# Kernel optimization log

Hardware: AMD Instinct MI355X
Metric: run time of the kernel (lower is better)

Reference implementation:

```python
import jax, jax.numpy as jnp
import numpy as np

N_NODES = 50000
N_EDGES = 250000
N_GRAPHS = 512
F_IN = 32
F_EDGE = 16
LATENT = 32
EMBED = 128


def setup_inputs() -> dict:
    key = jax.random.key(0)
    ks = jax.random.split(key, 10)
    x = jax.random.normal(ks[0], (N_NODES, F_IN), dtype=jnp.float32)
    edge_index = jax.random.randint(ks[1], (2, N_EDGES), 0, N_NODES, dtype=jnp.int64)
    edge_attr = jax.random.normal(ks[2], (N_EDGES, F_EDGE), dtype=jnp.float32)
    batch = jnp.sort(jax.random.randint(ks[3], (N_NODES,), 0, N_GRAPHS, dtype=jnp.int64))
    s = 0.05
    W1 = jax.random.normal(ks[4], (F_EDGE, LATENT), dtype=jnp.float32) * s
    b1 = jnp.zeros((LATENT,), jnp.float32)
    W2 = jax.random.normal(ks[5], (LATENT, F_IN * LATENT), dtype=jnp.float32) * s
    b2 = jnp.zeros((F_IN * LATENT,), jnp.float32)
    root = jax.random.normal(ks[6], (F_IN, LATENT), dtype=jnp.float32) * s
    conv_bias = jnp.zeros((LATENT,), jnp.float32)
    fc_w = jax.random.normal(ks[7], (LATENT, EMBED), dtype=jnp.float32) * s
    fc_b = jnp.zeros((EMBED,), jnp.float32)
    return dict(x=x, edge_index=edge_index, edge_attr=edge_attr, batch=batch,
                W1=W1, b1=b1, W2=W2, b2=b2, root=root, conv_bias=conv_bias,
                fc_w=fc_w, fc_b=fc_b)


def reference(x, edge_index, edge_attr, batch, W1, b1, W2, b2, root, conv_bias, fc_w, fc_b):
    src, dst = edge_index[0], edge_index[1]
    # edge MLP: [E, F_edge] -> [E, F_in*latent] -> [E, F_in, latent]
    h = jax.nn.relu(edge_attr @ W1 + b1)
    ew = (h @ W2 + b2).reshape(-1, F_IN, LATENT)
    # per-edge matvec: message_e = x[src_e] @ W_e
    msg = jnp.einsum('ef,efl->el', x[src], ew)
    # scatter-add to target nodes (NNConv default aggr='add')
    agg = jax.ops.segment_sum(msg, dst, num_segments=N_NODES)
    node = jax.nn.relu(agg + x @ root + conv_bias)
    # global mean pool per graph
    sums = jax.ops.segment_sum(node, batch, num_segments=N_GRAPHS)
    cnts = jax.ops.segment_sum(jnp.ones((node.shape[0],), node.dtype), batch, num_segments=N_GRAPHS)
    pooled = sums / jnp.maximum(cnts, 1.0)[:, None]
    return jax.nn.relu(pooled) @ fc_w + fc_b
```

## Files before the change

### kernel.cpp

```cpp
#include <hip/hip_runtime.h>
#include <hip/hip_fp16.h>

#define N_NODES 50000
#define N_EDGES 250000
#define N_GRAPHS 512
#define F_IN 32
#define F_EDGE 16
#define LATENT 32
#define EMBED 128
#define E_BLK 256
#define N_EBLK ((N_EDGES + E_BLK - 1) / E_BLK)
#define KW 1056
#define HS_STRIDE 36

typedef unsigned short ushort;
typedef unsigned int uint;
typedef _Float16 half8v __attribute__((ext_vector_type(8)));
typedef _Float16 half2v __attribute__((ext_vector_type(2)));
typedef __attribute__((ext_vector_type(4))) float f32x4;

union UH8 { half8v h8; half2v h2[4]; ushort u[8]; uint q[4]; };
union UH2 { half2v h2; uint q; };

__device__ inline ushort f2h_bits(float f) {
    _Float16 h = (_Float16)f;
    return *reinterpret_cast<ushort*>(&h);
}

__global__ void prep_kernel(const float* __restrict__ x, const float* __restrict__ W2,
                            const float* __restrict__ b2, ushort* __restrict__ xh,
                            ushort* __restrict__ W2T, uint4* __restrict__ aggz,
                            float* __restrict__ pool, float* __restrict__ pcnt) {
    int i = blockIdx.x * blockDim.x + threadIdx.x;
    if (i < (N_NODES * F_IN) / 4) {
        float4 v = ((const float4*)x)[i];
        union { ushort u[4]; uint2 q; } pk;
        pk.u[0] = f2h_bits(v.x); pk.u[1] = f2h_bits(v.y);
        pk.u[2] = f2h_bits(v.z); pk.u[3] = f2h_bits(v.w);
        ((uint2*)xh)[i] = pk.q;
    }
    if (i < (N_NODES * LATENT * 2) / 16) aggz[i] = make_uint4(0u, 0u, 0u, 0u);
    if (i < 32 * 1024) {
        int kk = i >> 5, l = i & 31;
        W2T[l * KW + kk] = f2h_bits(W2[i]);
    }
    if (i < 1024) {
        int f = i >> 5, l = i & 31;
        W2T[l * KW + 1024 + f] = f2h_bits(b2[i]);
    }
    if (i < N_GRAPHS * LATENT) pool[i] = 0.f;
    if (i < N_GRAPHS) pcnt[i] = 0.f;
}

__global__ __launch_bounds__(512) void edge_mfma_kernel(
    const ushort* __restrict__ xh, const int* __restrict__ ei,
    const float* __restrict__ ea, const float* __restrict__ W1,
    const float* __restrict__ b1, const ushort* __restrict__ W2T,
    __half* __restrict__ aggh)
{
    __shared__ __attribute__((aligned(16))) uint Hs2[E_BLK * HS_STRIDE];
    __shared__ __attribute__((aligned(16))) ushort W2q[32 * 256];

    const int t = threadIdx.x;
    const int e0 = blockIdx.x * E_BLK;
    const int wv = t >> 6, lane = t & 63;
    const int g = lane >> 4, j16 = lane & 15;

    UH8 bw[2];
    #pragma unroll
    for (int nt = 0; nt < 2; ++nt) {
        #pragma unroll
        for (int b = 0; b < 8; ++b) {
            float w = (g < 2) ? W1[(8 * g + b) * LATENT + nt * 16 + j16] : 0.f;
            bw[nt].u[b] = f2h_bits(w);
        }
    }
    float b1v[2] = { b1[j16], b1[16 + j16] };

    #pragma unroll
    for (int mt = 0; mt < 2; ++mt) {
        int mtg = 2 * wv + mt;
        int rowA = mtg * 16 + j16;
        int e = e0 + rowA; if (e >= N_EDGES) e = N_EDGES - 1;
        UH8 ae;
        if (g < 2) {
            const float4* p = (const float4*)(ea + (size_t)e * F_EDGE + 8 * g);
            float4 va = p[0], vb = p[1];
            ae.u[0] = f2h_bits(va.x); ae.u[1] = f2h_bits(va.y);
            ae.u[2] = f2h_bits(va.z); ae.u[3] = f2h_bits(va.w);
            ae.u[4] = f2h_bits(vb.x); ae.u[5] = f2h_bits(vb.y);
            ae.u[6] = f2h_bits(vb.z); ae.u[7] = f2h_bits(vb.w);
        } else {
            ae.q[0] = 0; ae.q[1] = 0; ae.q[2] = 0; ae.q[3] = 0;
        }
        #pragma unroll
        for (int nt = 0; nt < 2; ++nt) {
            f32x4 hacc = (f32x4){0.f, 0.f, 0.f, 0.f};
            hacc = __builtin_amdgcn_mfma_f32_16x16x32_f16(ae.h8, bw[nt].h8, hacc, 0, 0, 0);
            #pragma unroll
            for (int v = 0; v < 4; ++v) {
                int rowD = mtg * 16 + 4 * g + v;
                int col = nt * 16 + j16;
                float hval = fmaxf(hacc[v] + b1v[nt], 0.f);
                uint hb = (uint)f2h_bits(hval);
                Hs2[rowD * HS_STRIDE + col] = hb * 0x10001u;
            }
        }
    }
    if (t < E_BLK) Hs2[t * HS_STRIDE + 32] = 0x3C003C00u;

    f32x4 acc[2][2];
    #pragma unroll
    for (int a = 0; a < 2; ++a)
        #pragma unroll
        for (int b = 0; b < 2; ++b) acc[a][b] = (f32x4){0.f, 0.f, 0.f, 0.f};

    UH8 xf[2];
    int myrow[2];
    #pragma unroll
    for (int mt = 0; mt < 2; ++mt) {
        int row = (2 * wv + mt) * 16 + j16;
        myrow[mt] = row;
        int e = e0 + row; if (e >= N_EDGES) e = N_EDGES - 1;
        int src = ei[e];
        uint4 raw = *(const uint4*)(xh + (size_t)src * F_IN + 8 * g);
        xf[mt].q[0] = raw.x; xf[mt].q[1] = raw.y; xf[mt].q[2] = raw.z; xf[mt].q[3] = raw.w;
    }

    {
        UH8 bx0, bx1;
        *(uint4*)bx0.q = *(const uint4*)(W2T + (size_t)j16 * KW + 1024 + 8 * g);
        *(uint4*)bx1.q = *(const uint4*)(W2T + (size_t)(16 + j16) * KW + 1024 + 8 * g);
        #pragma unroll
        for (int mt = 0; mt < 2; ++mt) {
            acc[mt][0] = __builtin_amdgcn_mfma_f32_16x16x32_f16(xf[mt].h8, bx0.h8, acc[mt][0], 0, 0, 0);
            acc[mt][1] = __builtin_amdgcn_mfma_f32_16x16x32_f16(xf[mt].h8, bx1.h8, acc[mt][1], 0, 0, 0);
        }
    }

    __syncthreads();

    for (int q = 0; q < 4; ++q) {
        if (q) __syncthreads();
        #pragma unroll
        for (int c = 0; c < 2; ++c) {
            int ch = c * 512 + t;
            int lbyte = ch * 16;
            int jrow = lbyte >> 9;
            int off = lbyte & 511;
            uint4 val = *(const uint4*)((const char*)W2T + (size_t)jrow * (KW * 2) + q * 512 + off);
            *(uint4*)((char*)W2q + jrow * 512 + (off ^ ((jrow & 7) << 4))) = val;
        }
        __syncthreads();

        uint hb[2][8];
        #pragma unroll
        for (int mt = 0; mt < 2; ++mt) {
            const uint* hp = Hs2 + myrow[mt] * HS_STRIDE + q * 8;
            uint4 a = *(const uint4*)hp;
            uint4 b = *(const uint4*)(hp + 4);
            hb[mt][0] = a.x; hb[mt][1] = a.y; hb[mt][2] = a.z; hb[mt][3] = a.w;
            hb[mt][4] = b.x; hb[mt][5] = b.y; hb[mt][6] = b.z; hb[mt][7] = b.w;
        }

        #pragma unroll
        for (int kst = 0; kst < 8; ++kst) {
            int kb = kst * 64 + g * 16;
            UH8 bf0, bf1;
            *(uint4*)bf0.q = *(const uint4*)((const char*)W2q + j16 * 512 + (kb ^ ((j16 & 7) << 4)));
            *(uint4*)bf1.q = *(const uint4*)((const char*)W2q + (16 + j16) * 512 + (kb ^ ((j16 & 7) << 4)));
            #pragma unroll
            for (int mt = 0; mt < 2; ++mt) {
                UH2 h2; h2.q = hb[mt][kst];
                UH8 af;
                #pragma unroll
                for (int p = 0; p < 4; ++p) af.h2[p] = h2.h2 * xf[mt].h2[p];
                acc[mt][0] = __builtin_amdgcn_mfma_f32_16x16x32_f16(af.h8, bf0.h8, acc[mt][0], 0, 0, 0);
                acc[mt][1] = __builtin_amdgcn_mfma_f32_16x16x32_f16(af.h8, bf1.h8, acc[mt][1], 0, 0, 0);
            }
        }
    }

    const int odd = j16 & 1;
    #pragma unroll
    for (int mt = 0; mt < 2; ++mt) {
        int rowb = (2 * wv + mt) * 16 + 4 * g;
        #pragma unroll
        for (int v = 0; v < 4; ++v) {
            int e = e0 + rowb + v;
            float a0 = acc[mt][0][v], a1 = acc[mt][1][v];
            float p0 = __shfl_xor(a0, 1);
            float p1 = __shfl_xor(a1, 1);
            if (e < N_EDGES) {
                int dst = ei[N_EDGES + e];
                __half2 hv = odd ? __floats2half2_rn(p1, a1) : __floats2half2_rn(a0, p0);
                int col = odd ? (15 + j16) : j16;
                unsafeAtomicAdd((__half2*)(aggh + (size_t)dst * LATENT + col), hv);
            }
        }
    }
}

#define VN 8
__global__ __launch_bounds__(256) void nodepool_kernel(
    const float* __restrict__ x, const __half* __restrict__ aggh,
    const float* __restrict__ root, const float* __restrict__ cbias,
    const int* __restrict__ batch, float* __restrict__ pool,
    float* __restrict__ pcnt)
{
    int t = threadIdx.x;
    int l = t & 31;
    int stripe = t >> 5;
    int v0 = (blockIdx.x * 8 + stripe) * VN;
    float rc[F_IN];
    #pragma unroll
    for (int f = 0; f < F_IN; ++f) rc[f] = root[f * LATENT + l];
    float cbl = cbias[l];

    float sum = 0.f, cnt = 0.f;
    int gcur = -1;
    for (int i = 0; i < VN; ++i) {
        int v = v0 + i;
        if (v >= N_NODES) break;
        int g = batch[v];
        if (g != gcur) {
            if (gcur >= 0) {
                atomicAdd(&pool[gcur * LATENT + l], sum);
                if (l == 0) atomicAdd(&pcnt[gcur], cnt);
            }
            gcur = g; sum = 0.f; cnt = 0.f;
        }
        float xv = x[(size_t)v * F_IN + l];
        float a = __half2float(aggh[(size_t)v * LATENT + l]) + cbl;
        #pragma unroll
        for (int f = 0; f < F_IN; ++f) {
            float xfv = __shfl(xv, (t & 32) | f);
            a += xfv * rc[f];
        }
        sum += fmaxf(a, 0.f);
        cnt += 1.f;
    }
    if (gcur >= 0) {
        atomicAdd(&pool[gcur * LATENT + l], sum);
        if (l == 0) atomicAdd(&pcnt[gcur], cnt);
    }
}

__global__ void final_kernel(const float* __restrict__ pool, const float* __restrict__ pcnt,
                             const float* __restrict__ fcw, const float* __restrict__ fcb,
                             float* __restrict__ out)
{
    int t = blockIdx.x * blockDim.x + threadIdx.x;
    int gr = t >> 7, j = t & 127;
    if (gr >= N_GRAPHS) return;
    float inv = 1.0f / fmaxf(pcnt[gr], 1.0f);
    float o = fcb[j];
    #pragma unroll 8
    for (int l = 0; l < LATENT; ++l) {
        float pv = fmaxf(pool[gr * LATENT + l] * inv, 0.0f);
        o += pv * fcw[l * EMBED + j];
    }
    out[gr * EMBED + j] = o;
}

extern "C" void kernel_launch(void* const* d_in, const int* in_sizes, int n_in,
                              void* d_out, int out_size, void* d_ws, size_t ws_size,
                              hipStream_t stream)
{
    const float* x     = (const float*)d_in[0];
    const int*   ei    = (const int*)d_in[1];
    const float* ea    = (const float*)d_in[2];
    const int*   batch = (const int*)d_in[3];
    const float* W1    = (const float*)d_in[4];
    const float* b1    = (const float*)d_in[5];
    const float* W2    = (const float*)d_in[6];
    const float* b2    = (const float*)d_in[7];
    const float* root  = (const float*)d_in[8];
    const float* cb    = (const float*)d_in[9];
    const float* fcw   = (const float*)d_in[10];
    const float* fcb   = (const float*)d_in[11];
    float* out = (float*)d_out;

    char* w = (char*)d_ws;
    auto alloc = [&](size_t bytes) {
        char* p = w;
        w += (bytes + 255) & ~size_t(255);
        return p;
    };
    ushort* W2T  = (ushort*)alloc((size_t)32 * KW * 2);
    ushort* xh   = (ushort*)alloc((size_t)N_NODES * F_IN * 2);
    __half* aggh = (__half*)alloc((size_t)N_NODES * LATENT * 2);
    float*  pool = (float*)alloc(N_GRAPHS * LATENT * 4);
    float*  pcnt = (float*)alloc(N_GRAPHS * 4);

    prep_kernel<<<1563, 256, 0, stream>>>(x, W2, b2, xh, W2T, (uint4*)aggh, pool, pcnt);
    edge_mfma_kernel<<<N_EBLK, 512, 0, stream>>>(xh, ei, ea, W1, b1, W2T, aggh);
    nodepool_kernel<<<(N_NODES + 8 * VN - 1) / (8 * VN), 256, 0, stream>>>(
        x, aggh, root, cb, batch, pool, pcnt);
    final_kernel<<<(N_GRAPHS * EMBED + 255) / 256, 256, 0, stream>>>(pool, pcnt, fcw, fcb, out);
}
```

Baseline: 64.28 us.

## Prefetch W2 chunks into registers and shrink the H tile to half storage

The W2 chunk for the next iteration is loaded from global memory into registers while MFMAs run on the current chunk, then written to LDS after a barrier. The first chunk's load is issued at kernel start. This hides global load latency behind compute. The H tile now stores single halves instead of duplicated half2 words, which halves LDS usage and possibly raises occupancy, at the cost of a few extra bit-shuffle ops to rebuild the pairs.

```diff
diff --git a/kernel.cpp b/kernel.cpp
--- a/kernel.cpp
+++ b/kernel.cpp
@@ -11,7 +11,7 @@
 #define E_BLK 256
 #define N_EBLK ((N_EDGES + E_BLK - 1) / E_BLK)
 #define KW 1056
-#define HS_STRIDE 36
+#define HS_ST 36
 
 typedef unsigned short ushort;
 typedef unsigned int uint;
@@ -58,13 +58,21 @@
     const float* __restrict__ b1, const ushort* __restrict__ W2T,
     __half* __restrict__ aggh)
 {
-    __shared__ __attribute__((aligned(16))) uint Hs2[E_BLK * HS_STRIDE];
+    __shared__ __attribute__((aligned(16))) ushort Hs[E_BLK * HS_ST];
     __shared__ __attribute__((aligned(16))) ushort W2q[32 * 256];
 
     const int t = threadIdx.x;
     const int e0 = blockIdx.x * E_BLK;
     const int wv = t >> 6, lane = t & 63;
     const int g = lane >> 4, j16 = lane & 15;
+
+    uint4 st[2];
+    const int ch0 = t, ch1 = 512 + t;
+    const int jrow0 = (ch0 * 16) >> 9, off0 = (ch0 * 16) & 511;
+    const int jrow1 = (ch1 * 16) >> 9, off1 = (ch1 * 16) & 511;
+
+    st[0] = *(const uint4*)((const char*)W2T + (size_t)jrow0 * (KW * 2) + 0 * 512 + off0);
+    st[1] = *(const uint4*)((const char*)W2T + (size_t)jrow1 * (KW * 2) + 0 * 512 + off1);
 
     UH8 bw[2];
     #pragma unroll
@@ -102,12 +110,10 @@
                 int rowD = mtg * 16 + 4 * g + v;
                 int col = nt * 16 + j16;
                 float hval = fmaxf(hacc[v] + b1v[nt], 0.f);
-                uint hb = (uint)f2h_bits(hval);
-                Hs2[rowD * HS_STRIDE + col] = hb * 0x10001u;
-            }
-        }
-    }
-    if (t < E_BLK) Hs2[t * HS_STRIDE + 32] = 0x3C003C00u;
+                Hs[rowD * HS_ST + col] = f2h_bits(hval);
+            }
+        }
+    }
 
     f32x4 acc[2][2];
     #pragma unroll
@@ -138,29 +144,29 @@
         }
     }
 
+    *(uint4*)((char*)W2q + jrow0 * 512 + (off0 ^ ((jrow0 & 7) << 4))) = st[0];
+    *(uint4*)((char*)W2q + jrow1 * 512 + (off1 ^ ((jrow1 & 7) << 4))) = st[1];
     __syncthreads();
 
     for (int q = 0; q < 4; ++q) {
-        if (q) __syncthreads();
-        #pragma unroll
-        for (int c = 0; c < 2; ++c) {
-            int ch = c * 512 + t;
-            int lbyte = ch * 16;
-            int jrow = lbyte >> 9;
-            int off = lbyte & 511;
-            uint4 val = *(const uint4*)((const char*)W2T + (size_t)jrow * (KW * 2) + q * 512 + off);
-            *(uint4*)((char*)W2q + jrow * 512 + (off ^ ((jrow & 7) << 4))) = val;
-        }
-        __syncthreads();
-
-        uint hb[2][8];
+        if (q < 3) {
+            st[0] = *(const uint4*)((const char*)W2T + (size_t)jrow0 * (KW * 2) + (q + 1) * 512 + off0);
+            st[1] = *(const uint4*)((const char*)W2T + (size_t)jrow1 * (KW * 2) + (q + 1) * 512 + off1);
+        }
+
+        uint hbp[2][8];
         #pragma unroll
         for (int mt = 0; mt < 2; ++mt) {
-            const uint* hp = Hs2 + myrow[mt] * HS_STRIDE + q * 8;
-            uint4 a = *(const uint4*)hp;
-            uint4 b = *(const uint4*)(hp + 4);
-            hb[mt][0] = a.x; hb[mt][1] = a.y; hb[mt][2] = a.z; hb[mt][3] = a.w;
-            hb[mt][4] = b.x; hb[mt][5] = b.y; hb[mt][6] = b.z; hb[mt][7] = b.w;
+            const ushort* hp = Hs + myrow[mt] * HS_ST + q * 8;
+            uint2 ra = *(const uint2*)hp;
+            uint2 rb = *(const uint2*)(hp + 4);
+            uint raw[4] = { ra.x, ra.y, rb.x, rb.y };
+            #pragma unroll
+            for (int i = 0; i < 4; ++i) {
+                uint u = raw[i];
+                hbp[mt][2 * i]     = (u << 16) | (u & 0xFFFFu);
+                hbp[mt][2 * i + 1] = (u >> 16) | (u & 0xFFFF0000u);
+            }
         }
 
         #pragma unroll
@@ -171,13 +177,20 @@
             *(uint4*)bf1.q = *(const uint4*)((const char*)W2q + (16 + j16) * 512 + (kb ^ ((j16 & 7) << 4)));
             #pragma unroll
             for (int mt = 0; mt < 2; ++mt) {
-                UH2 h2; h2.q = hb[mt][kst];
+                UH2 h2; h2.q = hbp[mt][kst];
                 UH8 af;
                 #pragma unroll
                 for (int p = 0; p < 4; ++p) af.h2[p] = h2.h2 * xf[mt].h2[p];
                 acc[mt][0] = __builtin_amdgcn_mfma_f32_16x16x32_f16(af.h8, bf0.h8, acc[mt][0], 0, 0, 0);
                 acc[mt][1] = __builtin_amdgcn_mfma_f32_16x16x32_f16(af.h8, bf1.h8, acc[mt][1], 0, 0, 0);
             }
+        }
+
+        __syncthreads();
+        if (q < 3) {
+            *(uint4*)((char*)W2q + jrow0 * 512 + (off0 ^ ((jrow0 & 7) << 4))) = st[0];
+            *(uint4*)((char*)W2q + jrow1 * 512 + (off1 ^ ((jrow1 & 7) << 4))) = st[1];
+            __syncthreads();
         }
     }
 
```

Result: slower. 73.74 us (+14.7%).
